# Kernel tuning notes

Hardware: AMD Instinct MI355X
Metric: run time of the kernel (lower is better)

The kernel has to match this reference:

```python
import jax, jax.numpy as jnp
import numpy as np

VOCAB = 50257
SEQ = 2048  # == max_sentence_size; positional add requires seq == max_sentence_size
DIM = 768
BATCH = 8


def setup_inputs() -> dict:
    key = jax.random.key(0)
    k1, k2, k3 = jax.random.split(key, 3)
    tokens = jax.random.randint(k1, (BATCH, SEQ), 0, VOCAB, dtype=jnp.int32)
    # nn.Linear(vocab, d).weight has shape [d, vocab]
    W_emb = jax.random.normal(k2, (DIM, VOCAB), dtype=jnp.float32) * 0.02
    # nn.Linear(d, max_sentence).weight has shape [max_sentence, d]
    W_pos = jax.random.normal(k3, (SEQ, DIM), dtype=jnp.float32) * 0.02
    return {"tokens": tokens, "W_emb": W_emb, "W_pos": W_pos}


def reference(tokens, W_emb, W_pos):
    # Original: one_hot(tokens, vocab) @ W_emb.T  -- mathematically a gather
    # of rows of W_emb.T (= columns of W_emb). Expressed as an efficient take.
    tok_emb = jnp.take(W_emb.T, tokens, axis=0)  # (B, S, D)
    # Positional embedding broadcasts over batch: (S, D)
    return tok_emb + W_pos
```

## Files before the change

kernel.cpp:

```cpp
#include <hip/hip_runtime.h>

#define BATCH 8
#define SEQ   2048
#define DIM   768
#define VOCAB 50257
#define NTOK  (BATCH * SEQ)
#define NBUCKET 3142
#define OFF_BASE NTOK
#define SORT_THREADS 1024
#define LDS_PITCH 772

typedef float f32x4 __attribute__((ext_vector_type(4)));

__global__ __launch_bounds__(SORT_THREADS) void sort_tokens_kernel(
    const int* __restrict__ tokens, unsigned* __restrict__ ws)
{
    __shared__ unsigned cnt[4096];
    __shared__ unsigned wsum[16];
    const int tid = threadIdx.x;

    for (int j = tid; j < 4096; j += SORT_THREADS) cnt[j] = 0;
    __syncthreads();

    for (int i = tid; i < NTOK; i += SORT_THREADS) {
        int t = tokens[i];
        atomicAdd(&cnt[t >> 4], 1u);
    }
    __syncthreads();

    unsigned c0 = cnt[4*tid+0], c1 = cnt[4*tid+1], c2 = cnt[4*tid+2], c3 = cnt[4*tid+3];
    unsigned tsum = c0 + c1 + c2 + c3;
    unsigned x = tsum;
    for (int off = 1; off < 64; off <<= 1) {
        unsigned y = __shfl_up(x, off, 64);
        if ((tid & 63) >= off) x += y;
    }
    if ((tid & 63) == 63) wsum[tid >> 6] = x;
    __syncthreads();
    if (tid < 16) {
        unsigned w = wsum[tid];
        for (int off = 1; off < 16; off <<= 1) {
            unsigned y = __shfl_up(w, off, 64);
            if (tid >= off) w += y;
        }
        wsum[tid] = w;
    }
    __syncthreads();
    unsigned wavebase = (tid >= 64) ? wsum[(tid >> 6) - 1] : 0u;
    unsigned excl = wavebase + x - tsum;
    cnt[4*tid+0] = excl;
    cnt[4*tid+1] = excl + c0;
    cnt[4*tid+2] = excl + c0 + c1;
    cnt[4*tid+3] = excl + c0 + c1 + c2;
    __syncthreads();

    for (int j = tid; j < 4096; j += SORT_THREADS) ws[OFF_BASE + j] = cnt[j];
    __syncthreads();

    for (int i = tid; i < NTOK; i += SORT_THREADS) {
        int t = tokens[i];
        unsigned p = atomicAdd(&cnt[t >> 4], 1u);
        ws[p] = ((unsigned)t << 14) | (unsigned)i;
    }
}

__global__ __launch_bounds__(256) void emb_slab_kernel(
    const unsigned* __restrict__ ws,
    const float*    __restrict__ W_emb,
    const float*    __restrict__ W_pos,
    float*          __restrict__ out)
{
    __shared__ float slab[16 * LDS_PITCH];

    const int c = blockIdx.x;
    const unsigned start = ws[OFF_BASE + c];
    const unsigned end   = ws[OFF_BASE + c + 1];
    if (start == end) return;

    const int base = (16 * c <= VOCAB - 16) ? 16 * c : (VOCAB - 16);

    const int tid = threadIdx.x;
    const int q  = tid & 3;
    const int r0 = tid >> 2;

    f32x4 v[12];
    #pragma unroll
    for (int it = 0; it < 12; ++it) {
        const int r = r0 + it * 64;
        v[it] = *reinterpret_cast<const f32x4*>(W_emb + (size_t)r * VOCAB + base + 4 * q);
    }
    #pragma unroll
    for (int it = 0; it < 12; ++it) {
        const int r = r0 + it * 64;
        slab[(4*q + 0) * LDS_PITCH + r] = v[it].x;
        slab[(4*q + 1) * LDS_PITCH + r] = v[it].y;
        slab[(4*q + 2) * LDS_PITCH + r] = v[it].z;
        slab[(4*q + 3) * LDS_PITCH + r] = v[it].w;
    }
    __syncthreads();

    if (tid < 192) {
        const int d4 = tid * 4;
        for (unsigned idx = start; idx < end; ++idx) {
            const unsigned packed = ws[idx];
            const int t = (int)(packed >> 14);
            const int i = (int)(packed & 16383u);
            const int s = i & (SEQ - 1);
            const int j = t - base;

            const f32x4 col = *reinterpret_cast<const f32x4*>(&slab[j * LDS_PITCH + d4]);
            const f32x4 p   = *reinterpret_cast<const f32x4*>(W_pos + s * DIM + d4);
            const f32x4 rr  = col + p;
            __builtin_nontemporal_store(rr, reinterpret_cast<f32x4*>(out + (size_t)i * DIM + d4));
        }
    }
}

extern "C" void kernel_launch(void* const* d_in, const int* in_sizes, int n_in,
                              void* d_out, int out_size, void* d_ws, size_t ws_size,
                              hipStream_t stream) {
    const int*   tokens = (const int*)  d_in[0];
    const float* W_emb  = (const float*)d_in[1];
    const float* W_pos  = (const float*)d_in[2];
    float*       out    = (float*)d_out;
    unsigned*    ws     = (unsigned*)d_ws;

    sort_tokens_kernel<<<dim3(1), dim3(SORT_THREADS), 0, stream>>>(tokens, ws);
    emb_slab_kernel<<<dim3(NBUCKET), dim3(256), 0, stream>>>(ws, W_emb, W_pos, out);
}
```

Before: 270.6 us.

## Tile embedding gather into 128-column by 96-row panels with swizzled LDS

Each block now loads a 96-row by 128-column panel of W_emb, covering 8 vocab buckets and one eighth of the embedding dimension. The old design used a 16-column slab of all 768 rows per bucket. The wider panel gives more contiguous bytes per row read from W_emb (512B instead of 64B), aiming at better DRAM coalescing. LDS stores use an XOR swizzle to avoid bank conflicts. The output phase spreads tokens across all 256 threads rather than 192. The cost is 8 blocks per group, and each one rereads the token list and the W_pos rows.

```diff
diff --git a/kernel.cpp b/kernel.cpp
--- a/kernel.cpp
+++ b/kernel.cpp
@@ -6,9 +6,11 @@
 #define VOCAB 50257
 #define NTOK  (BATCH * SEQ)
 #define NBUCKET 3142
+#define NGROUP  393
 #define OFF_BASE NTOK
 #define SORT_THREADS 1024
-#define LDS_PITCH 772
+#define PCOLS 128
+#define PROWS 96
 
 typedef float f32x4 __attribute__((ext_vector_type(4)));
 
@@ -64,55 +66,77 @@
     }
 }
 
-__global__ __launch_bounds__(256) void emb_slab_kernel(
+__global__ __launch_bounds__(256) void emb_panel_kernel(
     const unsigned* __restrict__ ws,
     const float*    __restrict__ W_emb,
     const float*    __restrict__ W_pos,
     float*          __restrict__ out)
 {
-    __shared__ float slab[16 * LDS_PITCH];
+    __shared__ float slab[PROWS * PCOLS];
 
-    const int c = blockIdx.x;
-    const unsigned start = ws[OFF_BASE + c];
-    const unsigned end   = ws[OFF_BASE + c + 1];
+    const int b  = blockIdx.x;
+    const int G  = b >> 3;
+    const int rc = b & 7;
+    const unsigned start = ws[OFF_BASE + G * 8];
+    const unsigned end   = ws[OFF_BASE + G * 8 + 8];
     if (start == end) return;
 
-    const int base = (16 * c <= VOCAB - 16) ? 16 * c : (VOCAB - 16);
-
-    const int tid = threadIdx.x;
-    const int q  = tid & 3;
-    const int r0 = tid >> 2;
+    const int cbase = G * PCOLS;
+    const int rbase = rc * PROWS;
+    const int tid   = threadIdx.x;
 
     f32x4 v[12];
     #pragma unroll
     for (int it = 0; it < 12; ++it) {
-        const int r = r0 + it * 64;
-        v[it] = *reinterpret_cast<const f32x4*>(W_emb + (size_t)r * VOCAB + base + 4 * q);
+        const int f   = it * 1024 + tid * 4;
+        const int row = f >> 7;
+        const int col = f & 127;
+        const int gcol = cbase + col;
+        const float* src = W_emb + (size_t)(rbase + row) * VOCAB + gcol;
+        if (gcol + 4 <= VOCAB) {
+            v[it] = *reinterpret_cast<const f32x4*>(src);
+        } else {
+            f32x4 tmp = {0.f, 0.f, 0.f, 0.f};
+            #pragma unroll
+            for (int k = 0; k < 4; ++k)
+                if (gcol + k < VOCAB) tmp[k] = src[k];
+            v[it] = tmp;
+        }
     }
     #pragma unroll
     for (int it = 0; it < 12; ++it) {
-        const int r = r0 + it * 64;
-        slab[(4*q + 0) * LDS_PITCH + r] = v[it].x;
-        slab[(4*q + 1) * LDS_PITCH + r] = v[it].y;
-        slab[(4*q + 2) * LDS_PITCH + r] = v[it].z;
-        slab[(4*q + 3) * LDS_PITCH + r] = v[it].w;
+        const int f   = it * 1024 + tid * 4;
+        const int row = f >> 7;
+        const int col = f & 127;
+        const int colx = col ^ (((row >> 2) & 7) << 2);
+        *reinterpret_cast<f32x4*>(&slab[row * PCOLS + colx]) = v[it];
     }
     __syncthreads();
 
-    if (tid < 192) {
-        const int d4 = tid * 4;
-        for (unsigned idx = start; idx < end; ++idx) {
-            const unsigned packed = ws[idx];
-            const int t = (int)(packed >> 14);
-            const int i = (int)(packed & 16383u);
-            const int s = i & (SEQ - 1);
-            const int j = t - base;
+    const int ntok = (int)(end - start);
+    const int U = ntok * 24;
+    for (int u = tid; u < U; u += 256) {
+        const int tok = u / 24;
+        const int lp  = u - tok * 24;
+        const unsigned packed = ws[start + tok];
+        const int t = (int)(packed >> 14);
+        const int i = (int)(packed & 16383u);
+        const int s = i & (SEQ - 1);
+        const int j = t - cbase;
+        const int d0 = lp * 4;
 
-            const f32x4 col = *reinterpret_cast<const f32x4*>(&slab[j * LDS_PITCH + d4]);
-            const f32x4 p   = *reinterpret_cast<const f32x4*>(W_pos + s * DIM + d4);
-            const f32x4 rr  = col + p;
-            __builtin_nontemporal_store(rr, reinterpret_cast<f32x4*>(out + (size_t)i * DIM + d4));
+        float e[4];
+        #pragma unroll
+        for (int k = 0; k < 4; ++k) {
+            const int row = d0 + k;
+            e[k] = slab[row * PCOLS + (j ^ (((row >> 2) & 7) << 2))];
         }
+        const f32x4 p = *reinterpret_cast<const f32x4*>(
+            W_pos + (size_t)s * DIM + rbase + d0);
+        f32x4 rr;
+        rr.x = e[0] + p.x; rr.y = e[1] + p.y; rr.z = e[2] + p.z; rr.w = e[3] + p.w;
+        __builtin_nontemporal_store(rr,
+            reinterpret_cast<f32x4*>(out + (size_t)i * DIM + rbase + d0));
     }
 }
 
@@ -126,5 +150,5 @@
     unsigned*    ws     = (unsigned*)d_ws;
 
     sort_tokens_kernel<<<dim3(1), dim3(SORT_THREADS), 0, stream>>>(tokens, ws);
-    emb_slab_kernel<<<dim3(NBUCKET), dim3(256), 0, stream>>>(ws, W_emb, W_pos, out);
+    emb_panel_kernel<<<dim3(NGROUP * 8), dim3(256), 0, stream>>>(ws, W_emb, W_pos, out);
 }
```

Result: no change. 269.4 us (-0.4%).
